# Kernel tuning notes

Measured on AMD Instinct MI355X. Metric: run time of the kernel, lower is better.

Reference implementation:

```python
import jax, jax.numpy as jnp
import numpy as np

BEV_H, BEV_W = 496, 432  # cfg.bevshape

def mish(x):
    return x * jnp.tanh(jax.nn.softplus(x))

def ln(x, g, b, eps=1e-5):
    m = jnp.mean(x, axis=-1, keepdims=True)
    v = jnp.mean((x - m) ** 2, axis=-1, keepdims=True)
    return (x - m) * jax.lax.rsqrt(v + eps) * g + b

def fel(x, W, g, b):
    # FELayer: Linear(bias=False) -> LayerNorm -> Mish
    return mish(ln(x @ W.T, g, b))

def setup_inputs() -> dict:
    key = jax.random.key(0)
    ks = iter(jax.random.split(key, 48))
    Nv, P, Cin, Cv, Nb = 16000, 32, 10, 64, 16000
    inp = {}
    inp['voxels'] = jax.random.normal(next(ks), (Nv, P, Cin), jnp.float32)
    inp['voxelmask'] = jax.random.bernoulli(next(ks), 0.7, (Nv, P, 1)).astype(jnp.float32)
    inp['bevsidx'] = jax.random.randint(next(ks), (Nb, 64), 0, Nv, dtype=jnp.int32)
    flat = jax.random.choice(next(ks), BEV_H * BEV_W, (Nb,), replace=False)
    inp['bevcoors'] = jnp.stack([flat // BEV_W, flat % BEV_W], axis=1).astype(jnp.int32)
    inp['bevmask'] = jax.random.bernoulli(next(ks), 0.8, (Nb, 1, 1)).astype(jnp.float32)
    def w(shape):
        return jax.random.normal(next(ks), shape, jnp.float32) * 0.05
    for i, cin in zip((1, 2, 3, 4), (Cin, Cv, Cv, Cv)):
        inp[f'vfe{i}_W'] = w((Cv, cin))
        inp[f'vfe{i}_g'] = jnp.ones((Cv,), jnp.float32)
        inp[f'vfe{i}_b'] = jnp.zeros((Cv,), jnp.float32)
    inp['bfe1_W'] = w((16, Cv, Cv));  inp['bfe1_g'] = jnp.ones((16, Cv));  inp['bfe1_b'] = jnp.zeros((16, Cv))
    inp['bfe2a_W'] = w((16, 8, Cv)); inp['bfe2a_g'] = jnp.ones((16, 8));  inp['bfe2a_b'] = jnp.zeros((16, 8))
    inp['bfe2b_W'] = w((16, 8, 32)); inp['bfe2b_g'] = jnp.ones((16, 8));  inp['bfe2b_b'] = jnp.zeros((16, 8))
    inp['bfe3_W'] = w((128, 128));   inp['bfe3_g'] = jnp.ones((128,));   inp['bfe3_b'] = jnp.zeros((128,))
    return inp

def reference(voxels, voxelmask, bevsidx, bevcoors, bevmask,
              vfe1_W, vfe1_g, vfe1_b, vfe2_W, vfe2_g, vfe2_b,
              vfe3_W, vfe3_g, vfe3_b, vfe4_W, vfe4_g, vfe4_b,
              bfe1_W, bfe1_g, bfe1_b, bfe2a_W, bfe2a_g, bfe2a_b,
              bfe2b_W, bfe2b_g, bfe2b_b, bfe3_W, bfe3_g, bfe3_b):
    # voxel feature encoder with masked residual
    x1 = fel(voxels, vfe1_W, vfe1_g, vfe1_b)            # [Nv, P, 64]
    x2 = fel(x1, vfe2_W, vfe2_g, vfe2_b) * voxelmask
    x3 = fel(x2, vfe3_W, vfe3_g, vfe3_b)
    x4 = fel(x3, vfe4_W, vfe4_g, vfe4_b) * voxelmask + x2
    voxelwise = jnp.max(x4, axis=1)                     # [Nv, 64]
    # gather 64 voxels per BEV cell
    bevs = voxelwise[bevsidx]                           # [Nb, 64 voxels, 64 ch]
    x0 = jnp.transpose(bevs, (0, 2, 1))                 # [Nb, 64 ch, 64 voxels]
    Nb = x0.shape[0]
    xg = x0.reshape(Nb, 16, 4, 64)                      # 16 branches of 4 channel-rows
    # bfe1_k (vectorized over the 16 branches) + bev mask
    h = mish(ln(jnp.einsum('ngpc,goc->ngpo', xg, bfe1_W), bfe1_g[:, None, :], bfe1_b[:, None, :]))
    h = h * bevmask[:, None]                            # bevmask [Nb,1,1] -> broadcast
    # bfe2_k: NormalFELayer(in_points=4, in=64, out=8)
    h = mish(ln(jnp.einsum('ngpc,goc->ngpo', h, bfe2a_W), bfe2a_g[:, None, :], bfe2a_b[:, None, :]))
    h = h.reshape(Nb, 16, 32)
    h = mish(ln(jnp.einsum('ngc,goc->ngo', h, bfe2b_W), bfe2b_g, bfe2b_b))  # [Nb,16,8]
    x17 = h.reshape(Nb, 128)                            # cat of 16 branches
    x18 = fel(x17, bfe3_W, bfe3_g, bfe3_b)
    x19 = fel(x18, bfe3_W, bfe3_g, bfe3_b) + x17        # same bfe3 applied twice + residual
    bevmap = jnp.zeros((BEV_H, BEV_W, 128), jnp.float32).at[bevcoors[:, 0], bevcoors[:, 1]].set(x19)
    return jnp.transpose(bevmap, (2, 1, 0))             # [128, W, H]
```

## Files before the change

kernel.cpp:

```cpp
#include <hip/hip_runtime.h>
#include <math.h>

constexpr int NV  = 16000;
constexpr int P   = 32;
constexpr int CIN = 10;
constexpr int CV  = 64;
constexpr int NB  = 16000;
constexpr int BEV_H = 496, BEV_W = 432;
constexpr int HW = BEV_H * BEV_W;
constexpr float EPS = 1e-5f;

typedef __attribute__((ext_vector_type(8))) short short8_t;
typedef __attribute__((ext_vector_type(4))) short short4_t;
typedef __attribute__((ext_vector_type(4))) float fx4;
typedef __attribute__((ext_vector_type(2))) float f32x2;

__device__ __forceinline__ float mish(float x) {
  float e = __expf(fminf(x, 15.f));
  float u = 1.f + e;
  float d = fmaf(u, u, 1.f);
  float r = __builtin_amdgcn_rcpf(d);
  return fmaf(-2.f * x, r, x);
}

__device__ __forceinline__ short f2bf(float f) {
  unsigned u = __builtin_bit_cast(unsigned, f);
  u += 0x7FFF + ((u >> 16) & 1);
  return (short)(u >> 16);
}
__device__ __forceinline__ float bf2f(short s) {
  unsigned u = ((unsigned)(unsigned short)s) << 16;
  return __builtin_bit_cast(float, u);
}
__device__ __forceinline__ short8_t pack8(const float* t) {
  short8_t s;
#pragma unroll
  for (int j = 0; j < 8; ++j) s[j] = f2bf(t[j]);
  return s;
}

__device__ __forceinline__ unsigned bfpair(float a, float b) {
  unsigned au = __builtin_bit_cast(unsigned, a) + 0x8000u;
  unsigned bu = __builtin_bit_cast(unsigned, b) + 0x8000u;
  return __builtin_amdgcn_perm(bu, au, 0x07060302u);
}
__device__ __forceinline__ unsigned hipack(float a, float b, float& la, float& lb) {
  unsigned ua = (__builtin_bit_cast(unsigned, a) + 0x8000u) & 0xFFFF0000u;
  unsigned ub = (__builtin_bit_cast(unsigned, b) + 0x8000u) & 0xFFFF0000u;
  la = a - __builtin_bit_cast(float, ua);
  lb = b - __builtin_bit_cast(float, ub);
  return __builtin_amdgcn_perm(ub, ua, 0x07060302u);
}

__global__ __launch_bounds__(256) void pack_weights_kernel(
    const float* __restrict__ W1, const float* __restrict__ W2a,
    const float* __restrict__ W2b, const float* __restrict__ W3,
    short* __restrict__ w1h,
    short* __restrict__ w2ah,
    short* __restrict__ w2bh,
    short* __restrict__ w3h, short* __restrict__ w3l)
{
  int i = blockIdx.x * 256 + threadIdx.x;
  if (i < 65536) {
    w1h[i] = f2bf(W1[i]);
  } else if (i < 81920) {
    int j = i - 65536;
    int g = j >> 10, o = (j >> 6) & 15, c = j & 63;
    float v = (o < 8) ? W2a[(g * 8 + o) * 64 + c] : 0.f;
    w2ah[j] = f2bf(v);
  } else if (i < 90112) {
    int k = i - 81920;
    int g = k >> 9, o = (k >> 5) & 15, c = k & 31;
    float v = (o < 8) ? W2b[(g * 8 + o) * 32 + c] : 0.f;
    w2bh[k] = f2bf(v);
  } else if (i < 106496) {
    int j = i - 90112;
    float v = W3[j];
    short h = f2bf(v);
    w3h[j] = h; w3l[j] = f2bf(v - bf2f(h));
  }
}

__global__ __launch_bounds__(256, 4) void vfe_mfma5_kernel(
    const float* __restrict__ voxels, const float* __restrict__ vmask,
    const float* __restrict__ W1, const float* __restrict__ g1, const float* __restrict__ b1,
    const float* __restrict__ W2, const float* __restrict__ g2, const float* __restrict__ b2,
    const float* __restrict__ W3, const float* __restrict__ g3, const float* __restrict__ b3,
    const float* __restrict__ W4, const float* __restrict__ g4, const float* __restrict__ b4,
    unsigned short* __restrict__ voxelwise)
{
  __shared__ short wlds[28 * 512];
  __shared__ short actb[4][16 * 72];
  __shared__ float gblds[512];

  const int tid  = threadIdx.x;
  const int lane = tid & 63;
  const int w    = tid >> 6;
  const int p    = lane & 15;
  const int q    = lane >> 4;
  const int gw   = blockIdx.x * 4 + w;

  for (int k = tid; k < 512; k += 256) {
    int region = k >> 6, off = k & 63;
    const float* src =
        region == 0 ? g1 : region == 1 ? b1 :
        region == 2 ? g2 : region == 3 ? b2 :
        region == 4 ? g3 : region == 5 ? b3 :
        region == 6 ? g4 : b4;
    gblds[k] = src[off];
  }
  for (int s = w; s < 28; s += 4) {
    float t[8];
    if (s < 4) {
      const int f = s;
#pragma unroll
      for (int j = 0; j < 8; ++j) {
        int c = 8 * q + j;
        t[j] = (c < CIN) ? W1[(p + 16 * f) * CIN + c] : 0.f;
      }
    } else {
      const int l = (s - 4) >> 3, rem = (s - 4) & 7, ch = rem >> 2, f = rem & 3;
      const float* Wl = (l == 0) ? W2 : (l == 1) ? W3 : W4;
      const float* src = Wl + (p + 16 * f) * CV + 32 * ch + 8 * q;
#pragma unroll
      for (int j = 0; j < 8; ++j) t[j] = src[j];
    }
    *(short8_t*)&wlds[s * 512 + lane * 8] = pack8(t);
  }
  __syncthreads();

  short* mybuf = &actb[w][0];
  const fx4 zacc = {0.f, 0.f, 0.f, 0.f};
  const int srcLane = ((lane >> 2) & 3) * 16 + (((lane >> 4) & 3) << 2) + (lane & 3);

  for (int i = 0; i < 4; ++i) {
    const int v = gw * 4 + i;
    float chmax0 = 0.f, vmaxv = 0.f;

    for (int h = 0; h < 2; ++h) {
      const int ptbase = v * 32 + h * 16;
      const float m = vmask[ptbase + p];
      float x2r[16];
      float cur[16];

      {
        const float* xrow = voxels + (size_t)(ptbase + p) * CIN;
        float t[8] = {0.f, 0.f, 0.f, 0.f, 0.f, 0.f, 0.f, 0.f};
        if (q == 0) {
          float2 a = *(const float2*)(xrow + 0);
          float2 b = *(const float2*)(xrow + 2);
          float2 c = *(const float2*)(xrow + 4);
          float2 d = *(const float2*)(xrow + 6);
          t[0] = a.x; t[1] = a.y; t[2] = b.x; t[3] = b.y;
          t[4] = c.x; t[5] = c.y; t[6] = d.x; t[7] = d.y;
        } else if (q == 1) {
          float2 a = *(const float2*)(xrow + 8);
          t[0] = a.x; t[1] = a.y;
        }
        uint4 bu = make_uint4(bfpair(t[0], t[1]), bfpair(t[2], t[3]),
                              bfpair(t[4], t[5]), bfpair(t[6], t[7]));
        short8_t bfrag = __builtin_bit_cast(short8_t, bu);
        fx4 acc[4];
#pragma unroll
        for (int f = 0; f < 4; ++f) {
          short8_t af = *(short8_t*)&wlds[f * 512 + lane * 8];
          acc[f] = __builtin_amdgcn_mfma_f32_16x16x32_bf16(af, bfrag, zacc, 0, 0, 0);
        }
        f32x2 s1v = {0.f, 0.f}, s2v = {0.f, 0.f};
#pragma unroll
        for (int f = 0; f < 4; ++f) {
          f32x2 a01 = __builtin_shufflevector(acc[f], acc[f], 0, 1);
          f32x2 a23 = __builtin_shufflevector(acc[f], acc[f], 2, 3);
          s1v = s1v + a01 + a23;
          s2v = __builtin_elementwise_fma(a01, a01, s2v);
          s2v = __builtin_elementwise_fma(a23, a23, s2v);
        }
        float s1 = s1v[0] + s1v[1], s2 = s2v[0] + s2v[1];
        s1 += __shfl_xor(s1, 16); s1 += __shfl_xor(s1, 32);
        s2 += __shfl_xor(s2, 16); s2 += __shfl_xor(s2, 32);
        float mean = s1 * (1.f / 64.f);
        float rstd = rsqrtf(fmaf(-mean, mean, s2 * (1.f / 64.f)) + EPS);
        float ms = -mean * rstd;
#pragma unroll
        for (int f = 0; f < 4; ++f) {
          float4 gv = *(const float4*)&gblds[16 * f + 4 * q];
          float4 bv = *(const float4*)&gblds[64 + 16 * f + 4 * q];
          float go[4] = {gv.x, gv.y, gv.z, gv.w};
          float bo[4] = {bv.x, bv.y, bv.z, bv.w};
          float o[4];
#pragma unroll
          for (int r = 0; r < 4; ++r)
            o[r] = mish(fmaf(fmaf(acc[f][r], rstd, ms), go[r], bo[r]));
          *(uint2*)&mybuf[p * 72 + 4 * q + 16 * f] =
              make_uint2(bfpair(o[0], o[1]), bfpair(o[2], o[3]));
        }
      }

#pragma unroll 1
      for (int l = 0; l < 3; ++l) {
        short8_t bf0 = *(short8_t*)&mybuf[p * 72 + 8 * q];
        short8_t bf1 = *(short8_t*)&mybuf[p * 72 + 8 * q + 32];
        fx4 acc[4];
#pragma unroll
        for (int f = 0; f < 4; ++f) {
          short8_t a0 = *(short8_t*)&wlds[(4 + l * 8 + f) * 512 + lane * 8];
          short8_t a1 = *(short8_t*)&wlds[(4 + l * 8 + 4 + f) * 512 + lane * 8];
          fx4 a = __builtin_amdgcn_mfma_f32_16x16x32_bf16(a0, bf0, zacc, 0, 0, 0);
          acc[f] = __builtin_amdgcn_mfma_f32_16x16x32_bf16(a1, bf1, a, 0, 0, 0);
        }
        f32x2 s1v = {0.f, 0.f}, s2v = {0.f, 0.f};
#pragma unroll
        for (int f = 0; f < 4; ++f) {
          f32x2 a01 = __builtin_shufflevector(acc[f], acc[f], 0, 1);
          f32x2 a23 = __builtin_shufflevector(acc[f], acc[f], 2, 3);
          s1v = s1v + a01 + a23;
          s2v = __builtin_elementwise_fma(a01, a01, s2v);
          s2v = __builtin_elementwise_fma(a23, a23, s2v);
        }
        float s1 = s1v[0] + s1v[1], s2 = s2v[0] + s2v[1];
        s1 += __shfl_xor(s1, 16); s1 += __shfl_xor(s1, 32);
        s2 += __shfl_xor(s2, 16); s2 += __shfl_xor(s2, 32);
        float mean = s1 * (1.f / 64.f);
        float rstd = rsqrtf(fmaf(-mean, mean, s2 * (1.f / 64.f)) + EPS);
        float ms = -mean * rstd;
        const int gbbase = (l + 1) * 128;
#pragma unroll
        for (int f = 0; f < 4; ++f) {
          float4 gv = *(const float4*)&gblds[gbbase + 16 * f + 4 * q];
          float4 bv = *(const float4*)&gblds[gbbase + 64 + 16 * f + 4 * q];
          float go[4] = {gv.x, gv.y, gv.z, gv.w};
          float bo[4] = {bv.x, bv.y, bv.z, bv.w};
          if (l == 0) {
            float o[4];
#pragma unroll
            for (int r = 0; r < 4; ++r) {
              o[r] = mish(fmaf(fmaf(acc[f][r], rstd, ms), go[r], bo[r])) * m;
              x2r[f * 4 + r] = o[r];
            }
            *(uint2*)&mybuf[p * 72 + 4 * q + 16 * f] =
                make_uint2(bfpair(o[0], o[1]), bfpair(o[2], o[3]));
          } else if (l == 1) {
            float o[4];
#pragma unroll
            for (int r = 0; r < 4; ++r)
              o[r] = mish(fmaf(fmaf(acc[f][r], rstd, ms), go[r], bo[r]));
            *(uint2*)&mybuf[p * 72 + 4 * q + 16 * f] =
                make_uint2(bfpair(o[0], o[1]), bfpair(o[2], o[3]));
          } else {
#pragma unroll
            for (int r = 0; r < 4; ++r) {
              float t1 = fmaf(fmaf(acc[f][r], rstd, ms), go[r], bo[r]);
              cur[f * 4 + r] = fmaf(mish(t1), m, x2r[f * 4 + r]);
            }
          }
        }
      }

#pragma unroll
      for (int t = 0; t < 8; ++t) {
        float send = (lane & 8) ? cur[t] : cur[t + 8];
        float got  = __shfl_xor(send, 8);
        float mine = (lane & 8) ? cur[t + 8] : cur[t];
        cur[t] = fmaxf(mine, got);
      }
#pragma unroll
      for (int t = 0; t < 4; ++t) {
        float send = (lane & 4) ? cur[t] : cur[t + 4];
        float got  = __shfl_xor(send, 4);
        float mine = (lane & 4) ? cur[t + 4] : cur[t];
        cur[t] = fmaxf(mine, got);
      }
#pragma unroll
      for (int t = 0; t < 2; ++t) {
        float send = (lane & 2) ? cur[t] : cur[t + 2];
        float got  = __shfl_xor(send, 2);
        float mine = (lane & 2) ? cur[t + 2] : cur[t];
        cur[t] = fmaxf(mine, got);
      }
      {
        float send = (lane & 1) ? cur[0] : cur[1];
        float got  = __shfl_xor(send, 1);
        float mine = (lane & 1) ? cur[1] : cur[0];
        cur[0] = fmaxf(mine, got);
      }
      float hm = __shfl(cur[0], srcLane);
      if (h == 0) chmax0 = hm; else vmaxv = fmaxf(chmax0, hm);
    }
    unsigned uv = __builtin_bit_cast(unsigned, vmaxv) + 0x8000u;
    voxelwise[v * 64 + lane] = (unsigned short)(uv >> 16);
  }
}

constexpr int XS_CH   = 72;
constexpr int XS_CELL = 64 * 72 + 16;
constexpr int ACT_OFF = 4 * XS_CELL;
constexpr int ACT_WS  = 16 * 72;
constexpr int H2_OFF  = ACT_OFF + 4 * ACT_WS;
constexpr int H2_WS   = 16 * 40;
constexpr int X17_OFF = H2_OFF + 4 * H2_WS;
constexpr int SMEM_SHORTS = X17_OFF + 4 * 132 * 2;

__device__ __forceinline__ uint2 gather_transpose(uint2 u2, int bit0, int bit1) {
  float a0 = __builtin_bit_cast(float, u2.x << 16);
  float a1 = __builtin_bit_cast(float, u2.x & 0xFFFF0000u);
  float a2 = __builtin_bit_cast(float, u2.y << 16);
  float a3 = __builtin_bit_cast(float, u2.y & 0xFFFF0000u);
  float gv0 = bit0 ? a0 : a1, gv1 = bit0 ? a2 : a3;
  float r0 = __shfl_xor(gv0, 4), r1 = __shfl_xor(gv1, 4);
  float c0 = bit0 ? r0 : a0, c1 = bit0 ? a1 : r0;
  float c2 = bit0 ? r1 : a2, c3 = bit0 ? a3 : r1;
  float h0 = bit1 ? c0 : c2, h1 = bit1 ? c1 : c3;
  float s0 = __shfl_xor(h0, 8), s1 = __shfl_xor(h1, 8);
  float d0 = bit1 ? s0 : c0, d1 = bit1 ? s1 : c1;
  float d2 = bit1 ? c2 : s0, d3 = bit1 ? c3 : s1;
  return make_uint2(bfpair(d0, d1), bfpair(d2, d3));
}

__global__ __launch_bounds__(256, 3) void bfe12_mfma6_kernel(
    const unsigned short* __restrict__ voxelwise, const int* __restrict__ bevsidx,
    const float* __restrict__ bevmask,
    const short* __restrict__ w1h,
    const float* __restrict__ g1, const float* __restrict__ b1,
    const short* __restrict__ w2ah,
    const float* __restrict__ g2a, const float* __restrict__ b2a,
    const short* __restrict__ w2bh,
    const float* __restrict__ g2b, const float* __restrict__ b2b,
    float* __restrict__ x17buf)
{
  extern __shared__ short sm[];
  float* x17lds = (float*)&sm[X17_OFF];

  const int tid  = threadIdx.x;
  const int lane = tid & 63;
  const int w    = tid >> 6;
  const int r15  = lane & 15;
  const int q    = lane >> 4;
  const int cellbase = blockIdx.x * 4;

  const int chq   = lane & 3;
  const int v_loc = (lane >> 2) & 3;
  const int vblk  = lane >> 4;
  const int bit0  = v_loc & 1, bit1 = v_loc >> 1;

  int idxr[4];
#pragma unroll
  for (int vb = 0; vb < 4; ++vb)
    idxr[vb] = bevsidx[(cellbase + w) * 64 + 16 * vb + 4 * vblk + v_loc];

  {
    short* zh = &sm[H2_OFF + w * H2_WS];
    for (int i = lane; i < 480; i += 64) zh[160 + i] = 0;
  }

  uint2 raw[4][4];
#pragma unroll
  for (int vb = 0; vb < 4; ++vb)
#pragma unroll
    for (int js = 0; js < 4; ++js)
      raw[vb][js] = *(const uint2*)(voxelwise + (size_t)idxr[vb] * 64 +
                                    16 * js + 4 * chq);
#pragma unroll
  for (int js = 0; js < 4; ++js)
#pragma unroll
    for (int vb = 0; vb < 4; ++vb) {
      uint2 packed = gather_transpose(raw[vb][js], bit0, bit1);
      int addr = w * XS_CELL + (16 * js + 4 * chq + v_loc) * XS_CH +
                 16 * vb + 4 * vblk;
      *(uint2*)&sm[addr] = packed;
    }

  __syncthreads();

  const fx4 zacc = {0.f, 0.f, 0.f, 0.f};
  short* acth = &sm[ACT_OFF + w * ACT_WS];
  short* h2h  = &sm[H2_OFF + w * H2_WS];

#pragma unroll 1
  for (int j = 0; j < 4; ++j) {
    const int g = 4 * j + w;

    short8_t W1f[2][4];
#pragma unroll
    for (int c = 0; c < 2; ++c)
#pragma unroll
      for (int f = 0; f < 4; ++f) {
        int off = (g * 64 + r15 + 16 * f) * 64 + 32 * c + 8 * q;
        W1f[c][f] = *(const short8_t*)&w1h[off];
      }
    short8_t W2af[2];
#pragma unroll
    for (int c = 0; c < 2; ++c) {
      int off = (g * 16 + r15) * 64 + 32 * c + 8 * q;
      W2af[c] = *(const short8_t*)&w2ah[off];
    }
    short8_t W2bf;
    {
      int off = (g * 16 + r15) * 32 + 8 * q;
      W2bf = *(const short8_t*)&w2bh[off];
    }

    {
      const int cl = r15 >> 2, p = r15 & 3;
      const float bm = bevmask[cellbase + cl];

      int xaddr = cl * XS_CELL + (4 * g + p) * XS_CH;
      short8_t x0 = *(short8_t*)&sm[xaddr + 8 * q];
      short8_t x1 = *(short8_t*)&sm[xaddr + 32 + 8 * q];

      fx4 acc[4];
#pragma unroll
      for (int f = 0; f < 4; ++f) {
        fx4 a = __builtin_amdgcn_mfma_f32_16x16x32_bf16(W1f[0][f], x0, zacc, 0, 0, 0);
        acc[f] = __builtin_amdgcn_mfma_f32_16x16x32_bf16(W1f[1][f], x1, a, 0, 0, 0);
      }

      f32x2 s1v = {0.f, 0.f}, s2v = {0.f, 0.f};
#pragma unroll
      for (int f = 0; f < 4; ++f) {
        f32x2 a01 = __builtin_shufflevector(acc[f], acc[f], 0, 1);
        f32x2 a23 = __builtin_shufflevector(acc[f], acc[f], 2, 3);
        s1v = s1v + a01 + a23;
        s2v = __builtin_elementwise_fma(a01, a01, s2v);
        s2v = __builtin_elementwise_fma(a23, a23, s2v);
      }
      float s1 = s1v[0] + s1v[1], s2 = s2v[0] + s2v[1];
      s1 += __shfl_xor(s1, 16); s1 += __shfl_xor(s1, 32);
      s2 += __shfl_xor(s2, 16); s2 += __shfl_xor(s2, 32);
      float mean = s1 * (1.f / 64.f);
      float rstd = rsqrtf(fmaf(-mean, mean, s2 * (1.f / 64.f)) + EPS);
      float ms = -mean * rstd;

#pragma unroll
      for (int f = 0; f < 4; ++f) {
        float4 gv = *(const float4*)(g1 + g * 64 + 16 * f + 4 * q);
        float4 bv = *(const float4*)(b1 + g * 64 + 16 * f + 4 * q);
        float go[4] = {gv.x, gv.y, gv.z, gv.w};
        float bo[4] = {bv.x, bv.y, bv.z, bv.w};
        float o[4];
#pragma unroll
        for (int r = 0; r < 4; ++r)
          o[r] = mish(fmaf(fmaf(acc[f][r], rstd, ms), go[r], bo[r])) * bm;
        *(uint2*)&acth[r15 * 72 + 16 * f + 4 * q] =
            make_uint2(bfpair(o[0], o[1]), bfpair(o[2], o[3]));
      }

      short8_t a0 = *(short8_t*)&acth[r15 * 72 + 8 * q];
      short8_t a1 = *(short8_t*)&acth[r15 * 72 + 32 + 8 * q];
      fx4 a2 = __builtin_amdgcn_mfma_f32_16x16x32_bf16(W2af[0], a0, zacc, 0, 0, 0);
      a2 = __builtin_amdgcn_mfma_f32_16x16x32_bf16(W2af[1], a1, a2, 0, 0, 0);

      float sa = a2[0] + a2[1] + a2[2] + a2[3];
      float sb = fmaf(a2[0], a2[0], fmaf(a2[1], a2[1], fmaf(a2[2], a2[2], a2[3] * a2[3])));
      sa += __shfl_xor(sa, 16); sb += __shfl_xor(sb, 16);
      if (q < 2) {
        float mean2 = sa * 0.125f;
        float rstd2 = rsqrtf(fmaf(-mean2, mean2, sb * 0.125f) + EPS);
        float ms2 = -mean2 * rstd2;
        float4 gv = *(const float4*)(g2a + g * 8 + 4 * q);
        float4 bv = *(const float4*)(b2a + g * 8 + 4 * q);
        float go[4] = {gv.x, gv.y, gv.z, gv.w};
        float bo[4] = {bv.x, bv.y, bv.z, bv.w};
        float o[4];
#pragma unroll
        for (int r = 0; r < 4; ++r)
          o[r] = mish(fmaf(fmaf(a2[r], rstd2, ms2), go[r], bo[r]));
        *(uint2*)&h2h[cl * 40 + p * 8 + 4 * q] =
            make_uint2(bfpair(o[0], o[1]), bfpair(o[2], o[3]));
      }
    }

    {
      short8_t bh = *(short8_t*)&h2h[r15 * 40 + 8 * q];
      fx4 a3 = __builtin_amdgcn_mfma_f32_16x16x32_bf16(W2bf, bh, zacc, 0, 0, 0);

      float sa = a3[0] + a3[1] + a3[2] + a3[3];
      float sb = fmaf(a3[0], a3[0], fmaf(a3[1], a3[1], fmaf(a3[2], a3[2], a3[3] * a3[3])));
      sa += __shfl_xor(sa, 16); sb += __shfl_xor(sb, 16);
      if (q < 2 && r15 < 4) {
        float mean3 = sa * 0.125f;
        float rstd3 = rsqrtf(fmaf(-mean3, mean3, sb * 0.125f) + EPS);
        float ms3 = -mean3 * rstd3;
        float4 gv = *(const float4*)(g2b + g * 8 + 4 * q);
        float4 bv = *(const float4*)(b2b + g * 8 + 4 * q);
        float go[4] = {gv.x, gv.y, gv.z, gv.w};
        float bo[4] = {bv.x, bv.y, bv.z, bv.w};
        float4 outv;
        float* op = &outv.x;
#pragma unroll
        for (int r = 0; r < 4; ++r)
          op[r] = mish(fmaf(fmaf(a3[r], rstd3, ms3), go[r], bo[r]));
        *(float4*)&x17lds[r15 * 132 + g * 8 + 4 * q] = outv;
      }
    }
  }

  __syncthreads();
  if (tid < 128) {
    const int cell = tid >> 5;
    const int off  = (tid & 31) * 4;
    float4 vq = *(const float4*)&x17lds[cell * 132 + off];
    *(float4*)&x17buf[(size_t)(cellbase + cell) * 128 + off] = vq;
  }
}

__global__ __launch_bounds__(256, 3) void bfe3_mfma2_kernel(
    const float* __restrict__ x17buf, const int* __restrict__ bevcoors,
    const short* __restrict__ w3h, const short* __restrict__ w3l,
    const float* __restrict__ g3, const float* __restrict__ b3,
    float* __restrict__ out)
{
  __shared__ short x18h[4][16 * 136];
  __shared__ short x18l[4][16 * 136];

  const int tid  = threadIdx.x;
  const int lane = tid & 63;
  const int w    = tid >> 6;
  const int r15  = lane & 15;
  const int q    = lane >> 4;
  const int cell = blockIdx.x * 64 + w * 16 + r15;
  const float* xr = x17buf + (size_t)cell * 128;
  short* xh18 = &x18h[w][0];
  short* xl18 = &x18l[w][0];
  const fx4 zacc = {0.f, 0.f, 0.f, 0.f};

  short8_t xh[4], xl[4];
#pragma unroll
  for (int c = 0; c < 4; ++c) {
    const float* s = xr + 32 * c + 8 * q;
    float4 A = *(const float4*)s;
    float4 B = *(const float4*)(s + 4);
    float t[8] = {A.x, A.y, A.z, A.w, B.x, B.y, B.z, B.w};
    unsigned hu[4], lu[4];
#pragma unroll
    for (int jj = 0; jj < 4; ++jj) {
      float la, lb;
      hu[jj] = hipack(t[2 * jj], t[2 * jj + 1], la, lb);
      lu[jj] = bfpair(la, lb);
    }
    xh[c] = __builtin_bit_cast(short8_t, make_uint4(hu[0], hu[1], hu[2], hu[3]));
    xl[c] = __builtin_bit_cast(short8_t, make_uint4(lu[0], lu[1], lu[2], lu[3]));
  }

  fx4 acc[8];
#pragma unroll
  for (int f = 0; f < 8; ++f) {
    fx4 a = zacc;
#pragma unroll
    for (int c = 0; c < 4; ++c) {
      int off = (16 * f + r15) * 128 + 32 * c + 8 * q;
      short8_t Ah = *(const short8_t*)&w3h[off];
      short8_t Al = *(const short8_t*)&w3l[off];
      a = __builtin_amdgcn_mfma_f32_16x16x32_bf16(Ah, xh[c], a, 0, 0, 0);
      a = __builtin_amdgcn_mfma_f32_16x16x32_bf16(Ah, xl[c], a, 0, 0, 0);
      a = __builtin_amdgcn_mfma_f32_16x16x32_bf16(Al, xh[c], a, 0, 0, 0);
    }
    acc[f] = a;
  }
  {
    f32x2 s1v = {0.f, 0.f}, s2v = {0.f, 0.f};
#pragma unroll
    for (int f = 0; f < 8; ++f) {
      f32x2 a01 = __builtin_shufflevector(acc[f], acc[f], 0, 1);
      f32x2 a23 = __builtin_shufflevector(acc[f], acc[f], 2, 3);
      s1v = s1v + a01 + a23;
      s2v = __builtin_elementwise_fma(a01, a01, s2v);
      s2v = __builtin_elementwise_fma(a23, a23, s2v);
    }
    float s1 = s1v[0] + s1v[1], s2 = s2v[0] + s2v[1];
    s1 += __shfl_xor(s1, 16); s1 += __shfl_xor(s1, 32);
    s2 += __shfl_xor(s2, 16); s2 += __shfl_xor(s2, 32);
    float mean = s1 * (1.f / 128.f);
    float rstd = rsqrtf(fmaf(-mean, mean, s2 * (1.f / 128.f)) + EPS);
    float ms = -mean * rstd;
#pragma unroll
    for (int f = 0; f < 8; ++f) {
      float4 gv = *(const float4*)(g3 + 16 * f + 4 * q);
      float4 bv = *(const float4*)(b3 + 16 * f + 4 * q);
      float go[4] = {gv.x, gv.y, gv.z, gv.w};
      float bo[4] = {bv.x, bv.y, bv.z, bv.w};
      float o[4];
#pragma unroll
      for (int r = 0; r < 4; ++r)
        o[r] = mish(fmaf(fmaf(acc[f][r], rstd, ms), go[r], bo[r]));
      float la0, lb0, la1, lb1;
      unsigned h01 = hipack(o[0], o[1], la0, lb0);
      unsigned h23 = hipack(o[2], o[3], la1, lb1);
      *(uint2*)&xh18[r15 * 136 + 16 * f + 4 * q] = make_uint2(h01, h23);
      *(uint2*)&xl18[r15 * 136 + 16 * f + 4 * q] =
          make_uint2(bfpair(la0, lb0), bfpair(la1, lb1));
    }
  }

  short8_t yh[4], yl[4];
#pragma unroll
  for (int c = 0; c < 4; ++c) {
    yh[c] = *(short8_t*)&xh18[r15 * 136 + 32 * c + 8 * q];
    yl[c] = *(short8_t*)&xl18[r15 * 136 + 32 * c + 8 * q];
  }
#pragma unroll
  for (int f = 0; f < 8; ++f) {
    fx4 a = zacc;
#pragma unroll
    for (int c = 0; c < 4; ++c) {
      int off = (16 * f + r15) * 128 + 32 * c + 8 * q;
      short8_t Ah = *(const short8_t*)&w3h[off];
      short8_t Al = *(const short8_t*)&w3l[off];
      a = __builtin_amdgcn_mfma_f32_16x16x32_bf16(Ah, yh[c], a, 0, 0, 0);
      a = __builtin_amdgcn_mfma_f32_16x16x32_bf16(Ah, yl[c], a, 0, 0, 0);
      a = __builtin_amdgcn_mfma_f32_16x16x32_bf16(Al, yh[c], a, 0, 0, 0);
    }
    acc[f] = a;
  }
  {
    f32x2 s1v = {0.f, 0.f}, s2v = {0.f, 0.f};
#pragma unroll
    for (int f = 0; f < 8; ++f) {
      f32x2 a01 = __builtin_shufflevector(acc[f], acc[f], 0, 1);
      f32x2 a23 = __builtin_shufflevector(acc[f], acc[f], 2, 3);
      s1v = s1v + a01 + a23;
      s2v = __builtin_elementwise_fma(a01, a01, s2v);
      s2v = __builtin_elementwise_fma(a23, a23, s2v);
    }
    float s1 = s1v[0] + s1v[1], s2 = s2v[0] + s2v[1];
    s1 += __shfl_xor(s1, 16); s1 += __shfl_xor(s1, 32);
    s2 += __shfl_xor(s2, 16); s2 += __shfl_xor(s2, 32);
    float mean = s1 * (1.f / 128.f);
    float rstd = rsqrtf(fmaf(-mean, mean, s2 * (1.f / 128.f)) + EPS);
    float ms = -mean * rstd;

    int2 hw2 = *(const int2*)&bevcoors[cell * 2];
    const int base = hw2.y * BEV_H + hw2.x;
#pragma unroll
    for (int f = 0; f < 8; ++f) {
      float4 gv = *(const float4*)(g3 + 16 * f + 4 * q);
      float4 bv = *(const float4*)(b3 + 16 * f + 4 * q);
      float go[4] = {gv.x, gv.y, gv.z, gv.w};
      float bo[4] = {bv.x, bv.y, bv.z, bv.w};
      float4 R = *(const float4*)(xr + 16 * f + 4 * q);
      float Ra[4] = {R.x, R.y, R.z, R.w};
#pragma unroll
      for (int r = 0; r < 4; ++r) {
        float t1 = fmaf(fmaf(acc[f][r], rstd, ms), go[r], bo[r]);
        float val = mish(t1) + Ra[r];
        out[(size_t)(16 * f + 4 * q + r) * HW + base] = val;
      }
    }
  }
}

extern "C" void kernel_launch(void* const* d_in, const int* in_sizes, int n_in,
                              void* d_out, int out_size, void* d_ws, size_t ws_size,
                              hipStream_t stream) {
  const float* voxels   = (const float*)d_in[0];
  const float* vmask    = (const float*)d_in[1];
  const int*   bevsidx  = (const int*)d_in[2];
  const int*   bevcoors = (const int*)d_in[3];
  const float* bevmask  = (const float*)d_in[4];
  const float* vfe1_W = (const float*)d_in[5];
  const float* vfe1_g = (const float*)d_in[6];
  const float* vfe1_b = (const float*)d_in[7];
  const float* vfe2_W = (const float*)d_in[8];
  const float* vfe2_g = (const float*)d_in[9];
  const float* vfe2_b = (const float*)d_in[10];
  const float* vfe3_W = (const float*)d_in[11];
  const float* vfe3_g = (const float*)d_in[12];
  const float* vfe3_b = (const float*)d_in[13];
  const float* vfe4_W = (const float*)d_in[14];
  const float* vfe4_g = (const float*)d_in[15];
  const float* vfe4_b = (const float*)d_in[16];
  const float* bfe1_W  = (const float*)d_in[17];
  const float* bfe1_g  = (const float*)d_in[18];
  const float* bfe1_b  = (const float*)d_in[19];
  const float* bfe2a_W = (const float*)d_in[20];
  const float* bfe2a_g = (const float*)d_in[21];
  const float* bfe2a_b = (const float*)d_in[22];
  const float* bfe2b_W = (const float*)d_in[23];
  const float* bfe2b_g = (const float*)d_in[24];
  const float* bfe2b_b = (const float*)d_in[25];
  const float* bfe3_W  = (const float*)d_in[26];
  const float* bfe3_g  = (const float*)d_in[27];
  const float* bfe3_b  = (const float*)d_in[28];

  unsigned short* voxelwise = (unsigned short*)d_ws;
  float* x17buf = (float*)(voxelwise + (size_t)NV * 64);
  short* wbase  = (short*)(x17buf + (size_t)NB * 128);
  short* w1h  = wbase;
  short* w2ah = w1h + 65536;
  short* w2bh = w2ah + 16384;
  short* w3h  = w2bh + 8192;
  short* w3l  = w3h + 16384;
  float* out = (float*)d_out;

  hipMemsetAsync(d_out, 0, (size_t)out_size * sizeof(float), stream);

  pack_weights_kernel<<<(106496 + 255) / 256, 256, 0, stream>>>(
      bfe1_W, bfe2a_W, bfe2b_W, bfe3_W,
      w1h, w2ah, w2bh, w3h, w3l);

  vfe_mfma5_kernel<<<NV / 16, 256, 0, stream>>>(
      voxels, vmask,
      vfe1_W, vfe1_g, vfe1_b, vfe2_W, vfe2_g, vfe2_b,
      vfe3_W, vfe3_g, vfe3_b, vfe4_W, vfe4_g, vfe4_b,
      voxelwise);

  bfe12_mfma6_kernel<<<NB / 4, 256, SMEM_SHORTS * sizeof(short), stream>>>(
      voxelwise, bevsidx, bevmask,
      w1h, bfe1_g, bfe1_b,
      w2ah, bfe2a_g, bfe2a_b,
      w2bh, bfe2b_g, bfe2b_b,
      x17buf);

  bfe3_mfma2_kernel<<<NB / 64, 256, 0, stream>>>(
      x17buf, bevcoors, w3h, w3l, bfe3_g, bfe3_b, out);
}
```

Baseline: 424.7 us.

## Use 8 waves per block in bfe12 with XOR-swizzled LDS and direct stores

Result: slower. 438.8 us (+3.3%).

```diff
diff --git a/kernel.cpp b/kernel.cpp
--- a/kernel.cpp
+++ b/kernel.cpp
@@ -291,14 +291,10 @@
   }
 }
 
-constexpr int XS_CH   = 72;
-constexpr int XS_CELL = 64 * 72 + 16;
+constexpr int XS_CELL = 64 * 64 + 16;
 constexpr int ACT_OFF = 4 * XS_CELL;
 constexpr int ACT_WS  = 16 * 72;
-constexpr int H2_OFF  = ACT_OFF + 4 * ACT_WS;
-constexpr int H2_WS   = 16 * 40;
-constexpr int X17_OFF = H2_OFF + 4 * H2_WS;
-constexpr int SMEM_SHORTS = X17_OFF + 4 * 132 * 2;
+constexpr int SMEM_SHORTS = ACT_OFF + 8 * ACT_WS;
 
 __device__ __forceinline__ uint2 gather_transpose(uint2 u2, int bit0, int bit1) {
   float a0 = __builtin_bit_cast(float, u2.x << 16);
@@ -316,7 +312,7 @@
   return make_uint2(bfpair(d0, d1), bfpair(d2, d3));
 }
 
-__global__ __launch_bounds__(256, 3) void bfe12_mfma6_kernel(
+__global__ __launch_bounds__(512, 6) void bfe12_mfma7_kernel(
     const unsigned short* __restrict__ voxelwise, const int* __restrict__ bevsidx,
     const float* __restrict__ bevmask,
     const short* __restrict__ w1h,
@@ -327,8 +323,7 @@
     const float* __restrict__ g2b, const float* __restrict__ b2b,
     float* __restrict__ x17buf)
 {
-  extern __shared__ short sm[];
-  float* x17lds = (float*)&sm[X17_OFF];
+  __shared__ short sm[SMEM_SHORTS];
 
   const int tid  = threadIdx.x;
   const int lane = tid & 63;
@@ -341,31 +336,30 @@
   const int v_loc = (lane >> 2) & 3;
   const int vblk  = lane >> 4;
   const int bit0  = v_loc & 1, bit1 = v_loc >> 1;
-
-  int idxr[4];
-#pragma unroll
-  for (int vb = 0; vb < 4; ++vb)
-    idxr[vb] = bevsidx[(cellbase + w) * 64 + 16 * vb + 4 * vblk + v_loc];
-
-  {
-    short* zh = &sm[H2_OFF + w * H2_WS];
-    for (int i = lane; i < 480; i += 64) zh[160 + i] = 0;
-  }
-
-  uint2 raw[4][4];
-#pragma unroll
-  for (int vb = 0; vb < 4; ++vb)
+  const int gcell = w >> 1;
+  const int vb0   = (w & 1) * 2;
+
+  int idxr[2];
+#pragma unroll
+  for (int vi = 0; vi < 2; ++vi)
+    idxr[vi] = bevsidx[(cellbase + gcell) * 64 + 16 * (vb0 + vi) + 4 * vblk + v_loc];
+
+  uint2 raw[2][4];
+#pragma unroll
+  for (int vi = 0; vi < 2; ++vi)
 #pragma unroll
     for (int js = 0; js < 4; ++js)
-      raw[vb][js] = *(const uint2*)(voxelwise + (size_t)idxr[vb] * 64 +
+      raw[vi][js] = *(const uint2*)(voxelwise + (size_t)idxr[vi] * 64 +
                                     16 * js + 4 * chq);
 #pragma unroll
   for (int js = 0; js < 4; ++js)
 #pragma unroll
-    for (int vb = 0; vb < 4; ++vb) {
-      uint2 packed = gather_transpose(raw[vb][js], bit0, bit1);
-      int addr = w * XS_CELL + (16 * js + 4 * chq + v_loc) * XS_CH +
-                 16 * vb + 4 * vblk;
+    for (int vi = 0; vi < 2; ++vi) {
+      uint2 packed = gather_transpose(raw[vi][js], bit0, bit1);
+      const int vb    = vb0 + vi;
+      const int ch    = 16 * js + 4 * chq + v_loc;
+      const int chunk = (2 * vb + (vblk >> 1)) ^ (ch & 7);
+      const int addr  = gcell * XS_CELL + ch * 64 + 8 * chunk + 4 * (vblk & 1);
       *(uint2*)&sm[addr] = packed;
     }
 
@@ -373,11 +367,13 @@
 
   const fx4 zacc = {0.f, 0.f, 0.f, 0.f};
   short* acth = &sm[ACT_OFF + w * ACT_WS];
-  short* h2h  = &sm[H2_OFF + w * H2_WS];
+  short* h2h  = acth;
+  const int cl = r15 >> 2, p = r15 & 3;
+  const float bm = bevmask[cellbase + cl];
 
 #pragma unroll 1
-  for (int j = 0; j < 4; ++j) {
-    const int g = 4 * j + w;
+  for (int j = 0; j < 2; ++j) {
+    const int g = 8 * j + w;
 
     short8_t W1f[2][4];
 #pragma unroll
@@ -400,12 +396,11 @@
     }
 
     {
-      const int cl = r15 >> 2, p = r15 & 3;
-      const float bm = bevmask[cellbase + cl];
-
-      int xaddr = cl * XS_CELL + (4 * g + p) * XS_CH;
-      short8_t x0 = *(short8_t*)&sm[xaddr + 8 * q];
-      short8_t x1 = *(short8_t*)&sm[xaddr + 32 + 8 * q];
+      const int ch    = 4 * g + p;
+      const int sw    = ch & 7;
+      const int xbase = cl * XS_CELL + ch * 64;
+      short8_t x0 = *(short8_t*)&sm[xbase + 8 * (q ^ sw)];
+      short8_t x1 = *(short8_t*)&sm[xbase + 8 * ((4 + q) ^ sw)];
 
       fx4 acc[4];
 #pragma unroll
@@ -446,6 +441,9 @@
 
       short8_t a0 = *(short8_t*)&acth[r15 * 72 + 8 * q];
       short8_t a1 = *(short8_t*)&acth[r15 * 72 + 32 + 8 * q];
+
+      if (lane < 60) *(uint2*)&h2h[160 + 8 * lane] = make_uint2(0u, 0u);
+
       fx4 a2 = __builtin_amdgcn_mfma_f32_16x16x32_bf16(W2af[0], a0, zacc, 0, 0, 0);
       a2 = __builtin_amdgcn_mfma_f32_16x16x32_bf16(W2af[1], a1, a2, 0, 0, 0);
 
@@ -489,17 +487,9 @@
 #pragma unroll
         for (int r = 0; r < 4; ++r)
           op[r] = mish(fmaf(fmaf(a3[r], rstd3, ms3), go[r], bo[r]));
-        *(float4*)&x17lds[r15 * 132 + g * 8 + 4 * q] = outv;
-      }
-    }
-  }
-
-  __syncthreads();
-  if (tid < 128) {
-    const int cell = tid >> 5;
-    const int off  = (tid & 31) * 4;
-    float4 vq = *(const float4*)&x17lds[cell * 132 + off];
-    *(float4*)&x17buf[(size_t)(cellbase + cell) * 128 + off] = vq;
+        *(float4*)&x17buf[(size_t)(cellbase + r15) * 128 + g * 8 + 4 * q] = outv;
+      }
+    }
   }
 }
 
@@ -703,7 +693,7 @@
       vfe3_W, vfe3_g, vfe3_b, vfe4_W, vfe4_g, vfe4_b,
       voxelwise);
 
-  bfe12_mfma6_kernel<<<NB / 4, 256, SMEM_SHORTS * sizeof(short), stream>>>(
+  bfe12_mfma7_kernel<<<NB / 4, 512, 0, stream>>>(
       voxelwise, bevsidx, bevmask,
       w1h, bfe1_g, bfe1_b,
       w2ah, bfe2a_g, bfe2a_b,
```
